# Performance work log

Measured on AMD Instinct MI355X. Metric: run time of the kernel, lower is better.

Reference implementation:

```python
import jax, jax.numpy as jnp
import numpy as np
from jax import lax

B, T, V, E, H = 4096, 80, 10000, 100, 64


def setup_inputs() -> dict:
    key = jax.random.key(0)
    ks = jax.random.split(key, 8)
    return {
        "tokens": jax.random.randint(ks[0], (B, T), 0, V, dtype=jnp.int32),
        "emb": jax.random.normal(ks[1], (V, E), jnp.float32) * 0.05,
        "Wx0": jax.random.normal(ks[2], (E, H), jnp.float32) * (1.0 / np.sqrt(E)),
        "Wh0": jax.random.normal(ks[3], (H, H), jnp.float32) * (1.0 / np.sqrt(H)),
        "b0": jnp.zeros((H,), jnp.float32),
        "Wx1": jax.random.normal(ks[4], (H, H), jnp.float32) * (1.0 / np.sqrt(H)),
        "Wh1": jax.random.normal(ks[5], (H, H), jnp.float32) * (1.0 / np.sqrt(H)),
        "b1": jnp.zeros((H,), jnp.float32),
        "Wout": jax.random.normal(ks[6], (H, 1), jnp.float32) * (1.0 / np.sqrt(H)),
        "bout": jnp.zeros((1,), jnp.float32),
    }


def reference(tokens, emb, Wx0, Wh0, b0, Wx1, Wh1, b1, Wout, bout):
    # Embedding lookup: [B, T, E]
    x = emb[tokens]
    batch = x.shape[0]
    h0 = jnp.zeros((batch, Wh0.shape[0]), x.dtype)
    h1 = jnp.zeros((batch, Wh1.shape[0]), x.dtype)

    def step(carry, xt):
        h0, h1 = carry
        # SimpleRNNCell: h = tanh(x @ Wx + h_prev @ Wh + b)  (dropout off in eval)
        h0 = jnp.tanh(xt @ Wx0 + h0 @ Wh0 + b0)
        h1 = jnp.tanh(h0 @ Wx1 + h1 @ Wh1 + b1)
        return (h0, h1), None

    # scan over time: xs has shape [T, B, E]
    (h0, h1), _ = lax.scan(step, (h0, h1), jnp.swapaxes(x, 0, 1))
    logits = h1 @ Wout + bout  # [B, 1]
    return jax.nn.sigmoid(logits)
```

## Files before the change

kernel.cpp:

```cpp
#include <hip/hip_runtime.h>

#define BB 4096
#define TT 80
#define VV 10000
#define EE 100
#define HH 64
#define STR 68
#define STRP 68

typedef _Float16 f16x8 __attribute__((ext_vector_type(8)));
typedef _Float16 f16x4 __attribute__((ext_vector_type(4)));
typedef __attribute__((ext_vector_type(4))) float f4v;

#define MFMA(w, s, c) __builtin_amdgcn_mfma_f32_16x16x32_f16((w), (s), (c), 0, 0, 0)

#define BAR() do { asm volatile("s_waitcnt lgkmcnt(0)" ::: "memory"); \
                   __builtin_amdgcn_s_barrier();                      \
                   asm volatile("" ::: "memory"); } while (0)

__device__ __forceinline__ float fast_tanh(float x) {
    float e = __builtin_amdgcn_exp2f(x * 2.8853900817779268f);
    return 1.0f - 2.0f * __builtin_amdgcn_rcpf(e + 1.0f);
}

__device__ __forceinline__ void load_wfrag(const float* __restrict__ W, int kf, int g,
                                           int c, f16x8& hi, f16x8& lo) {
    union { _Float16 h[8]; f16x8 v; } th, tl;
#pragma unroll
    for (int i = 0; i < 8; ++i) {
        float wv = W[(32 * kf + 8 * g + i) * HH + c];
        _Float16 hf = (_Float16)wv;
        th.h[i] = hf;
        tl.h[i] = (_Float16)(wv - (float)hf);
    }
    hi = th.v;
    lo = tl.v;
}

__global__ __launch_bounds__(256) void emb2_kernel(const float* __restrict__ emb,
                                                   const float* __restrict__ Wx0,
                                                   const float* __restrict__ b0,
                                                   _Float16* __restrict__ emb2h) {
    const int tid = threadIdx.x;
    const int wid = tid >> 6;
    const int l = tid & 63;
    const int g = l >> 4;
    const int r16 = l & 15;
    const int c = 16 * wid + r16;
    const int jcol = 16 * wid + 4 * g;
    const int vr = blockIdx.x * 16 + r16;

    f16x8 wa[4];
#pragma unroll
    for (int kf = 0; kf < 4; ++kf) {
        union { _Float16 h[8]; f16x8 v; } t;
#pragma unroll
        for (int i = 0; i < 8; ++i) {
            int e = 32 * kf + 8 * g + i;
            t.h[i] = (e < EE) ? (_Float16)Wx0[e * HH + c] : (_Float16)0.f;
        }
        wa[kf] = t.v;
    }
    const float* er = emb + (size_t)vr * EE;
    f4v acc = *(const f4v*)&b0[jcol];
#pragma unroll
    for (int kf = 0; kf < 4; ++kf) {
        union { _Float16 h[8]; f16x8 v; } tb;
#pragma unroll
        for (int i = 0; i < 8; ++i) {
            int e = 32 * kf + 8 * g + i;
            tb.h[i] = (e < EE) ? (_Float16)er[e] : (_Float16)0.f;
        }
        acc = MFMA(wa[kf], tb.v, acc);
    }
    f16x4 o;
#pragma unroll
    for (int q = 0; q < 4; ++q) o[q] = (_Float16)acc[q];
    *(f16x4*)&emb2h[(size_t)vr * HH + jcol] = o;
}

__global__ __launch_bounds__(768, 1) void rnn_pipe(
    const int* __restrict__ tokens, const _Float16* __restrict__ emb2,
    const float* __restrict__ Wh0, const float* __restrict__ Wx1,
    const float* __restrict__ Wh1, const float* __restrict__ b1,
    const float* __restrict__ Wout, const float* __restrict__ bout,
    float* __restrict__ out) {
    __shared__ __align__(16) _Float16 H0[2][16][STR];
    __shared__ __align__(16) _Float16 H1[2][16][STR];
    __shared__ __align__(16) float PP[2][16][STRP];
    __shared__ __align__(16) int tokT[TT][16];
    __shared__ float Pred[4][16];

    const int tid = threadIdx.x;
    const int w12 = tid >> 6;
    const int l = tid & 63;
    const int g = l >> 4;
    const int r16 = l & 15;
    const int role = w12 >> 2;
    const int tile = w12 & 3;
    const int c = 16 * tile + r16;
    const int jcol = 16 * tile + 4 * g;
    const int R = blockIdx.x * 16;

    for (int i = tid; i < 16 * TT; i += 768) {
        int r = i / TT, t = i - r * TT;
        tokT[t][r] = tokens[R * TT + i] << 7;
    }

    const float* Wsel = (role == 0) ? Wh0 : (role == 1 ? Wx1 : Wh1);
    f16x8 wAh[2], wAl[2];
    load_wfrag(Wsel, 0, g, c, wAh[0], wAl[0]);
    load_wfrag(Wsel, 1, g, c, wAh[1], wAl[1]);
    const f4v b1v = *(const f4v*)&b1[jcol];
    const f4v wov = *(const f4v*)&Wout[jcol];
    const f4v z4 = {0.f, 0.f, 0.f, 0.f};
    const char* ebase = (const char*)emb2 + (size_t)jcol * 2;

    BAR();

    f16x8 as0 = (f16x8)0, as1 = (f16x8)0;
    f16x4 xc = (f16x4)0, xn = (f16x4)0;

    if (role == 0) {
        xc = *(const f16x4*)(ebase + tokT[0][r16]);
        xn = *(const f16x4*)(ebase + tokT[1][r16]);
        f16x4 ph;
#pragma unroll
        for (int q = 0; q < 4; ++q) ph[q] = (_Float16)fast_tanh((float)xc[q]);
        *(f16x4*)&H0[0][r16][jcol] = ph;
        xc = xn;
    }
    BAR();
    if (role != 2) {
        as0 = *(const f16x8*)&H0[0][r16][8 * g];
        as1 = *(const f16x8*)&H0[0][r16][32 + 8 * g];
    }

#pragma unroll 2
    for (int q = 1; q <= 80; ++q) {
        const int par = q & 1;
        if (role == 0) {
            if (q <= TT - 1) {
                int pn = (q + 1 <= TT - 1) ? q + 1 : TT - 1;
                xn = *(const f16x4*)(ebase + tokT[pn][r16]);
                f4v C1 = {(float)xc[0], (float)xc[1], (float)xc[2], (float)xc[3]};
                C1 = MFMA(wAh[0], as0, C1);
                C1 = MFMA(wAh[1], as1, C1);
                f4v C2 = MFMA(wAl[0], as0, z4);
                C2 = MFMA(wAl[1], as1, C2);
                f4v acc = C1 + C2;
                f16x4 ph;
#pragma unroll
                for (int u = 0; u < 4; ++u) ph[u] = (_Float16)fast_tanh(acc[u]);
                *(f16x4*)&H0[par][r16][jcol] = ph;
                xc = xn;
            }
        } else if (role == 1) {
            f4v C1 = b1v;
            C1 = MFMA(wAh[0], as0, C1);
            C1 = MFMA(wAh[1], as1, C1);
            f4v C2 = MFMA(wAl[0], as0, z4);
            C2 = MFMA(wAl[1], as1, C2);
            f4v P = C1 + C2;
            *(f4v*)&PP[par][r16][jcol] = P;
        } else {
            if (q >= 2) {
                f4v C1 = *(const f4v*)&PP[par ^ 1][r16][jcol];
                C1 = MFMA(wAh[0], as0, C1);
                C1 = MFMA(wAh[1], as1, C1);
                f4v C2 = MFMA(wAl[0], as0, z4);
                C2 = MFMA(wAl[1], as1, C2);
                f4v acc = C1 + C2;
                f16x4 ph;
#pragma unroll
                for (int u = 0; u < 4; ++u) ph[u] = (_Float16)fast_tanh(acc[u]);
                *(f16x4*)&H1[par][r16][jcol] = ph;
            }
        }
        BAR();
        if (role != 2) {
            if (q <= TT - 1) {
                as0 = *(const f16x8*)&H0[par][r16][8 * g];
                as1 = *(const f16x8*)&H0[par][r16][32 + 8 * g];
            }
        } else {
            if (q >= 2) {
                as0 = *(const f16x8*)&H1[par][r16][8 * g];
                as1 = *(const f16x8*)&H1[par][r16][32 + 8 * g];
            }
        }
    }

    if (role == 2) {
        f4v C1 = *(const f4v*)&PP[0][r16][jcol];
        C1 = MFMA(wAh[0], as0, C1);
        C1 = MFMA(wAh[1], as1, C1);
        f4v C2 = MFMA(wAl[0], as0, z4);
        C2 = MFMA(wAl[1], as1, C2);
        f4v acc = C1 + C2;
        float pp = fast_tanh(acc[0]) * wov[0];
        pp = fmaf(fast_tanh(acc[1]), wov[1], pp);
        pp = fmaf(fast_tanh(acc[2]), wov[2], pp);
        pp = fmaf(fast_tanh(acc[3]), wov[3], pp);
        pp += __shfl_xor(pp, 16, 64);
        pp += __shfl_xor(pp, 32, 64);
        if (l < 16) Pred[tile][l] = pp;
    }
    BAR();
    if (tid < 16) {
        float logit = Pred[0][tid] + Pred[1][tid] + Pred[2][tid] +
                      Pred[3][tid] + bout[0];
        out[R + tid] = __builtin_amdgcn_rcpf(
            1.0f + __builtin_amdgcn_exp2f(-1.4426950408889634f * logit));
    }
}

extern "C" void kernel_launch(void* const* d_in, const int* in_sizes, int n_in,
                              void* d_out, int out_size, void* d_ws, size_t ws_size,
                              hipStream_t stream) {
    const int*   tokens = (const int*)  d_in[0];
    const float* emb    = (const float*)d_in[1];
    const float* Wx0    = (const float*)d_in[2];
    const float* Wh0    = (const float*)d_in[3];
    const float* b0     = (const float*)d_in[4];
    const float* Wx1    = (const float*)d_in[5];
    const float* Wh1    = (const float*)d_in[6];
    const float* b1     = (const float*)d_in[7];
    const float* Wout   = (const float*)d_in[8];
    const float* bout   = (const float*)d_in[9];
    float* out  = (float*)d_out;
    _Float16* emb2h = (_Float16*)d_ws;

    emb2_kernel<<<VV / 16, 256, 0, stream>>>(emb, Wx0, b0, emb2h);
    rnn_pipe<<<BB / 16, 768, 0, stream>>>(tokens, emb2h, Wh0, Wx1, Wh1, b1,
                                          Wout, bout, out);
}
```

Before: 42.59 us.

## Run each RNN layer recurrence in a single wave with register-resident state

Replaces the 12-wave role split, which needed a block barrier every timestep, with 4 waves. One wave runs the whole layer-0 recurrence and one runs the whole layer-1 recurrence. The hidden state stays in registers through a permuted weight-fragment layout, so each step's MFMA output feeds the next step's input without going through LDS. Two extra waves compute the Wx1 projection, and barriers now come only every 4 timesteps through ring buffers in shared memory. Each recurrent wave does four times the MFMA work per step serially, and the kernel launches fewer threads per block.

```diff
diff --git a/kernel.cpp b/kernel.cpp
--- a/kernel.cpp
+++ b/kernel.cpp
@@ -5,12 +5,11 @@
 #define VV 10000
 #define EE 100
 #define HH 64
-#define STR 68
-#define STRP 68
 
 typedef _Float16 f16x8 __attribute__((ext_vector_type(8)));
 typedef _Float16 f16x4 __attribute__((ext_vector_type(4)));
 typedef __attribute__((ext_vector_type(4))) float f4v;
+typedef __attribute__((ext_vector_type(4))) unsigned u4v;
 
 #define MFMA(w, s, c) __builtin_amdgcn_mfma_f32_16x16x32_f16((w), (s), (c), 0, 0, 0)
 
@@ -23,12 +22,13 @@
     return 1.0f - 2.0f * __builtin_amdgcn_rcpf(e + 1.0f);
 }
 
-__device__ __forceinline__ void load_wfrag(const float* __restrict__ W, int kf, int g,
-                                           int c, f16x8& hi, f16x8& lo) {
+__device__ __forceinline__ void load_wfrag_pi(const float* __restrict__ W, int kf,
+                                              int g, int c, f16x8& hi, f16x8& lo) {
     union { _Float16 h[8]; f16x8 v; } th, tl;
 #pragma unroll
     for (int i = 0; i < 8; ++i) {
-        float wv = W[(32 * kf + 8 * g + i) * HH + c];
+        int k = 16 * (i >> 1) + 4 * g + 2 * kf + (i & 1);
+        float wv = W[k * HH + c];
         _Float16 hf = (_Float16)wv;
         th.h[i] = hf;
         tl.h[i] = (_Float16)(wv - (float)hf);
@@ -79,139 +79,200 @@
     *(f16x4*)&emb2h[(size_t)vr * HH + jcol] = o;
 }
 
-__global__ __launch_bounds__(768, 1) void rnn_pipe(
+__global__ __launch_bounds__(256, 1) void rnn_pipe(
     const int* __restrict__ tokens, const _Float16* __restrict__ emb2,
     const float* __restrict__ Wh0, const float* __restrict__ Wx1,
     const float* __restrict__ Wh1, const float* __restrict__ b1,
     const float* __restrict__ Wout, const float* __restrict__ bout,
     float* __restrict__ out) {
-    __shared__ __align__(16) _Float16 H0[2][16][STR];
-    __shared__ __align__(16) _Float16 H1[2][16][STR];
-    __shared__ __align__(16) float PP[2][16][STRP];
-    __shared__ __align__(16) int tokT[TT][16];
-    __shared__ float Pred[4][16];
+    __shared__ __align__(16) unsigned HR[8][16 * 36];
+    __shared__ __align__(16) float    PR[8][4 * 16 * 20];
+    __shared__ int tokB[TT][16];
 
     const int tid = threadIdx.x;
-    const int w12 = tid >> 6;
+    const int wid = tid >> 6;
     const int l = tid & 63;
     const int g = l >> 4;
     const int r16 = l & 15;
-    const int role = w12 >> 2;
-    const int tile = w12 & 3;
-    const int c = 16 * tile + r16;
-    const int jcol = 16 * tile + 4 * g;
     const int R = blockIdx.x * 16;
 
-    for (int i = tid; i < 16 * TT; i += 768) {
+    for (int i = tid; i < 16 * TT; i += 256) {
         int r = i / TT, t = i - r * TT;
-        tokT[t][r] = tokens[R * TT + i] << 7;
-    }
-
-    const float* Wsel = (role == 0) ? Wh0 : (role == 1 ? Wx1 : Wh1);
-    f16x8 wAh[2], wAl[2];
-    load_wfrag(Wsel, 0, g, c, wAh[0], wAl[0]);
-    load_wfrag(Wsel, 1, g, c, wAh[1], wAl[1]);
-    const f4v b1v = *(const f4v*)&b1[jcol];
-    const f4v wov = *(const f4v*)&Wout[jcol];
+        tokB[t][r] = tokens[R * TT + i] << 7;
+    }
+
     const f4v z4 = {0.f, 0.f, 0.f, 0.f};
-    const char* ebase = (const char*)emb2 + (size_t)jcol * 2;
-
-    BAR();
-
-    f16x8 as0 = (f16x8)0, as1 = (f16x8)0;
-    f16x4 xc = (f16x4)0, xn = (f16x4)0;
-
-    if (role == 0) {
-        xc = *(const f16x4*)(ebase + tokT[0][r16]);
-        xn = *(const f16x4*)(ebase + tokT[1][r16]);
-        f16x4 ph;
-#pragma unroll
-        for (int q = 0; q < 4; ++q) ph[q] = (_Float16)fast_tanh((float)xc[q]);
-        *(f16x4*)&H0[0][r16][jcol] = ph;
-        xc = xn;
-    }
-    BAR();
-    if (role != 2) {
-        as0 = *(const f16x8*)&H0[0][r16][8 * g];
-        as1 = *(const f16x8*)&H0[0][r16][32 + 8 * g];
-    }
-
+    const char* ebase = (const char*)emb2;
+    const int hrW = r16 * 36 + g * 4;
+
+    if (wid == 0) {
+        f16x8 wh[4][2], wl[4][2];
+#pragma unroll
+        for (int t = 0; t < 4; ++t) {
+            int c = 16 * t + r16;
+            load_wfrag_pi(Wh0, 0, g, c, wh[t][0], wl[t][0]);
+            load_wfrag_pi(Wh0, 1, g, c, wh[t][1], wl[t][1]);
+        }
+        BAR();
+        f16x8 f0 = (f16x8)0, f1 = (f16x8)0;
+        f16x4 xb[2][4][4];
+#pragma unroll
+        for (int s = 0; s < 4; ++s) {
+            int tb = tokB[s][r16];
+#pragma unroll
+            for (int t = 0; t < 4; ++t)
+                xb[0][s][t] = *(const f16x4*)(ebase + tb + (16 * t + 4 * g) * 2);
+        }
 #pragma unroll 2
-    for (int q = 1; q <= 80; ++q) {
-        const int par = q & 1;
-        if (role == 0) {
-            if (q <= TT - 1) {
-                int pn = (q + 1 <= TT - 1) ? q + 1 : TT - 1;
-                xn = *(const f16x4*)(ebase + tokT[pn][r16]);
-                f4v C1 = {(float)xc[0], (float)xc[1], (float)xc[2], (float)xc[3]};
-                C1 = MFMA(wAh[0], as0, C1);
-                C1 = MFMA(wAh[1], as1, C1);
-                f4v C2 = MFMA(wAl[0], as0, z4);
-                C2 = MFMA(wAl[1], as1, C2);
-                f4v acc = C1 + C2;
-                f16x4 ph;
-#pragma unroll
-                for (int u = 0; u < 4; ++u) ph[u] = (_Float16)fast_tanh(acc[u]);
-                *(f16x4*)&H0[par][r16][jcol] = ph;
-                xc = xn;
-            }
-        } else if (role == 1) {
-            f4v C1 = b1v;
-            C1 = MFMA(wAh[0], as0, C1);
-            C1 = MFMA(wAh[1], as1, C1);
-            f4v C2 = MFMA(wAl[0], as0, z4);
-            C2 = MFMA(wAl[1], as1, C2);
-            f4v P = C1 + C2;
-            *(f4v*)&PP[par][r16][jcol] = P;
-        } else {
-            if (q >= 2) {
-                f4v C1 = *(const f4v*)&PP[par ^ 1][r16][jcol];
-                C1 = MFMA(wAh[0], as0, C1);
-                C1 = MFMA(wAh[1], as1, C1);
-                f4v C2 = MFMA(wAl[0], as0, z4);
-                C2 = MFMA(wAl[1], as1, C2);
-                f4v acc = C1 + C2;
-                f16x4 ph;
-#pragma unroll
-                for (int u = 0; u < 4; ++u) ph[u] = (_Float16)fast_tanh(acc[u]);
-                *(f16x4*)&H1[par][r16][jcol] = ph;
-            }
-        }
+        for (int Wg = 0; Wg < 22; ++Wg) {
+            if (Wg + 1 < 20) {
+#pragma unroll
+                for (int s = 0; s < 4; ++s) {
+                    int tb = tokB[4 * (Wg + 1) + s][r16];
+#pragma unroll
+                    for (int t = 0; t < 4; ++t)
+                        xb[(Wg + 1) & 1][s][t] =
+                            *(const f16x4*)(ebase + tb + (16 * t + 4 * g) * 2);
+                }
+            }
+            if (Wg < 20) {
+#pragma unroll
+                for (int s = 0; s < 4; ++s) {
+                    const int p = 4 * Wg + s;
+                    f4v acc[4];
+#pragma unroll
+                    for (int t = 0; t < 4; ++t) {
+                        f16x4 xr = xb[Wg & 1][s][t];
+                        f4v A1 = {(float)xr[0], (float)xr[1],
+                                  (float)xr[2], (float)xr[3]};
+                        A1 = MFMA(wh[t][0], f0, A1);
+                        A1 = MFMA(wh[t][1], f1, A1);
+                        f4v A2 = MFMA(wl[t][0], f0, z4);
+                        A2 = MFMA(wl[t][1], f1, A2);
+                        acc[t] = A1 + A2;
+                    }
+                    union { _Float16 h[8]; f16x8 v; u4v u; } p0, p1;
+#pragma unroll
+                    for (int t = 0; t < 4; ++t) {
+                        p0.h[2 * t]     = (_Float16)fast_tanh(acc[t][0]);
+                        p0.h[2 * t + 1] = (_Float16)fast_tanh(acc[t][1]);
+                        p1.h[2 * t]     = (_Float16)fast_tanh(acc[t][2]);
+                        p1.h[2 * t + 1] = (_Float16)fast_tanh(acc[t][3]);
+                    }
+                    f0 = p0.v; f1 = p1.v;
+                    const int sl = p & 7;
+                    *(u4v*)&HR[sl][hrW]      = p0.u;
+                    *(u4v*)&HR[sl][hrW + 16] = p1.u;
+                }
+            }
+            BAR();
+        }
+    } else if (wid == 1) {
+        f16x8 wh[4][2], wl[4][2];
+        f4v wov[4];
+#pragma unroll
+        for (int t = 0; t < 4; ++t) {
+            int c = 16 * t + r16;
+            load_wfrag_pi(Wh1, 0, g, c, wh[t][0], wl[t][0]);
+            load_wfrag_pi(Wh1, 1, g, c, wh[t][1], wl[t][1]);
+            wov[t] = *(const f4v*)&Wout[16 * t + 4 * g];
+        }
+        const float bo = bout[0];
         BAR();
-        if (role != 2) {
-            if (q <= TT - 1) {
-                as0 = *(const f16x8*)&H0[par][r16][8 * g];
-                as1 = *(const f16x8*)&H0[par][r16][32 + 8 * g];
-            }
-        } else {
-            if (q >= 2) {
-                as0 = *(const f16x8*)&H1[par][r16][8 * g];
-                as1 = *(const f16x8*)&H1[par][r16][32 + 8 * g];
-            }
-        }
-    }
-
-    if (role == 2) {
-        f4v C1 = *(const f4v*)&PP[0][r16][jcol];
-        C1 = MFMA(wAh[0], as0, C1);
-        C1 = MFMA(wAh[1], as1, C1);
-        f4v C2 = MFMA(wAl[0], as0, z4);
-        C2 = MFMA(wAl[1], as1, C2);
-        f4v acc = C1 + C2;
-        float pp = fast_tanh(acc[0]) * wov[0];
-        pp = fmaf(fast_tanh(acc[1]), wov[1], pp);
-        pp = fmaf(fast_tanh(acc[2]), wov[2], pp);
-        pp = fmaf(fast_tanh(acc[3]), wov[3], pp);
+        f16x8 f0 = (f16x8)0, f1 = (f16x8)0;
+        float vv[4][4] = {};
+#pragma unroll 2
+        for (int Wg = 0; Wg < 22; ++Wg) {
+            if (Wg >= 2) {
+                f4v pr[4][4];
+#pragma unroll
+                for (int s = 0; s < 4; ++s) {
+                    const int sl = (4 * (Wg - 2) + s) & 7;
+#pragma unroll
+                    for (int t = 0; t < 4; ++t)
+                        pr[s][t] = *(const f4v*)&PR[sl][(t * 16 + r16) * 20 + g * 4];
+                }
+#pragma unroll
+                for (int s = 0; s < 4; ++s) {
+                    f4v acc[4];
+#pragma unroll
+                    for (int t = 0; t < 4; ++t) {
+                        f4v A1 = pr[s][t];
+                        A1 = MFMA(wh[t][0], f0, A1);
+                        A1 = MFMA(wh[t][1], f1, A1);
+                        f4v A2 = MFMA(wl[t][0], f0, z4);
+                        A2 = MFMA(wl[t][1], f1, A2);
+                        acc[t] = A1 + A2;
+                    }
+                    union { _Float16 h[8]; f16x8 v; } p0, p1;
+#pragma unroll
+                    for (int t = 0; t < 4; ++t) {
+                        vv[t][0] = fast_tanh(acc[t][0]);
+                        vv[t][1] = fast_tanh(acc[t][1]);
+                        vv[t][2] = fast_tanh(acc[t][2]);
+                        vv[t][3] = fast_tanh(acc[t][3]);
+                        p0.h[2 * t]     = (_Float16)vv[t][0];
+                        p0.h[2 * t + 1] = (_Float16)vv[t][1];
+                        p1.h[2 * t]     = (_Float16)vv[t][2];
+                        p1.h[2 * t + 1] = (_Float16)vv[t][3];
+                    }
+                    f0 = p0.v; f1 = p1.v;
+                }
+            }
+            BAR();
+        }
+        float pp = 0.f;
+#pragma unroll
+        for (int t = 0; t < 4; ++t)
+#pragma unroll
+            for (int q = 0; q < 4; ++q)
+                pp = fmaf(vv[t][q], wov[t][q], pp);
         pp += __shfl_xor(pp, 16, 64);
         pp += __shfl_xor(pp, 32, 64);
-        if (l < 16) Pred[tile][l] = pp;
-    }
-    BAR();
-    if (tid < 16) {
-        float logit = Pred[0][tid] + Pred[1][tid] + Pred[2][tid] +
-                      Pred[3][tid] + bout[0];
-        out[R + tid] = __builtin_amdgcn_rcpf(
-            1.0f + __builtin_amdgcn_exp2f(-1.4426950408889634f * logit));
+        if (l < 16) {
+            float logit = pp + bo;
+            out[R + l] = __builtin_amdgcn_rcpf(
+                1.0f + __builtin_amdgcn_exp2f(-1.4426950408889634f * logit));
+        }
+    } else {
+        const int t0 = 2 * (wid - 2);
+        f16x8 wxh[2][2], wxl[2][2];
+        f4v b1v[2];
+#pragma unroll
+        for (int tt = 0; tt < 2; ++tt) {
+            int c = 16 * (t0 + tt) + r16;
+            load_wfrag_pi(Wx1, 0, g, c, wxh[tt][0], wxl[tt][0]);
+            load_wfrag_pi(Wx1, 1, g, c, wxh[tt][1], wxl[tt][1]);
+            b1v[tt] = *(const f4v*)&b1[16 * (t0 + tt) + 4 * g];
+        }
+        BAR();
+#pragma unroll 2
+        for (int Wg = 0; Wg < 22; ++Wg) {
+            if (Wg >= 1 && Wg <= 20) {
+                f16x8 fr0[4], fr1[4];
+#pragma unroll
+                for (int s = 0; s < 4; ++s) {
+                    const int sl = (4 * (Wg - 1) + s) & 7;
+                    fr0[s] = *(const f16x8*)&HR[sl][hrW];
+                    fr1[s] = *(const f16x8*)&HR[sl][hrW + 16];
+                }
+#pragma unroll
+                for (int s = 0; s < 4; ++s) {
+                    const int sl = (4 * (Wg - 1) + s) & 7;
+#pragma unroll
+                    for (int tt = 0; tt < 2; ++tt) {
+                        f4v C1 = b1v[tt];
+                        C1 = MFMA(wxh[tt][0], fr0[s], C1);
+                        C1 = MFMA(wxh[tt][1], fr1[s], C1);
+                        f4v C2 = MFMA(wxl[tt][0], fr0[s], z4);
+                        C2 = MFMA(wxl[tt][1], fr1[s], C2);
+                        f4v P = C1 + C2;
+                        *(f4v*)&PR[sl][((t0 + tt) * 16 + r16) * 20 + g * 4] = P;
+                    }
+                }
+            }
+            BAR();
+        }
     }
 }
 
@@ -232,6 +293,6 @@
     _Float16* emb2h = (_Float16*)d_ws;
 
     emb2_kernel<<<VV / 16, 256, 0, stream>>>(emb, Wx0, b0, emb2h);
-    rnn_pipe<<<BB / 16, 768, 0, stream>>>(tokens, emb2h, Wh0, Wx1, Wh1, b1,
+    rnn_pipe<<<BB / 16, 256, 0, stream>>>(tokens, emb2h, Wh0, Wx1, Wh1, b1,
                                           Wout, bout, out);
 }
```

Measured after the change: 59.88 us. +40.6%, slower.
